# Optimization experiments

Hardware: AMD Instinct MI355X
Metric: run time of the kernel (lower is better)

The kernel has to match this reference:

```python
import jax, jax.numpy as jnp
import numpy as np

B, T, OB, AC, OBL, ACL, W = 2048, 128, 64, 8, 32, 16, 64
DT = 0.05   # spacing of save times
K = 2       # fixed Dopri5 substeps per interval (step size = ode_dt0 = 0.025)


def _mlp2(x, W0, b0, W1, b1):
    # eqx.nn.MLP with depth=1: in -> width (relu) -> out (identity)
    return jax.nn.relu(x @ W0.T + b0) @ W1.T + b1


def setup_inputs() -> dict:
    key = jax.random.key(0)
    ks = jax.random.split(key, 10)
    def lin(k, o, i, scale=1.0):
        return (jax.random.normal(k, (o, i), jnp.float32) * (scale / np.sqrt(i))).astype(jnp.float32)
    return {
        "encW0": lin(ks[0], W, OB), "encb0": jnp.zeros((W,), jnp.float32),
        "encW1": lin(ks[1], OBL, W), "encb1": jnp.zeros((OBL,), jnp.float32),
        "acW0": lin(ks[2], W, AC), "acb0": jnp.zeros((W,), jnp.float32),
        "acW1": lin(ks[3], ACL, W), "acb1": jnp.zeros((ACL,), jnp.float32),
        "dynW0": lin(ks[4], W, OBL + ACL), "dynb0": jnp.zeros((W,), jnp.float32),
        "dynW1": lin(ks[5], OBL, W, 0.5), "dynb1": jnp.zeros((OBL,), jnp.float32),
        "decW0": lin(ks[6], W, OBL), "decb0": jnp.zeros((W,), jnp.float32),
        "decW1": lin(ks[7], OB, W), "decb1": jnp.zeros((OB,), jnp.float32),
        "ob": jax.random.normal(ks[8], (B, OB), jnp.float32),
        "acs": jax.random.normal(ks[9], (B, T, AC), jnp.float32),
        "times": jnp.tile(jnp.arange(T, dtype=jnp.float32) * DT, (B, 1)),
    }


def _dopri5_step(f, t, y, h):
    k1 = f(t, y)
    k2 = f(t + h * (1. / 5.), y + h * ((1. / 5.) * k1))
    k3 = f(t + h * (3. / 10.), y + h * ((3. / 40.) * k1 + (9. / 40.) * k2))
    k4 = f(t + h * (4. / 5.), y + h * ((44. / 45.) * k1 - (56. / 15.) * k2 + (32. / 9.) * k3))
    k5 = f(t + h * (8. / 9.), y + h * ((19372. / 6561.) * k1 - (25360. / 2187.) * k2
                                       + (64448. / 6561.) * k3 - (212. / 729.) * k4))
    k6 = f(t + h, y + h * ((9017. / 3168.) * k1 - (355. / 33.) * k2 + (46732. / 5247.) * k3
                           + (49. / 176.) * k4 - (5103. / 18656.) * k5))
    return y + h * ((35. / 384.) * k1 + (500. / 1113.) * k3 + (125. / 192.) * k4
                    - (2187. / 6784.) * k5 + (11. / 84.) * k6)


def reference(encW0, encb0, encW1, encb1, acW0, acb0, acW1, acb1,
              dynW0, dynb0, dynW1, dynb1, decW0, decb0, decW1, decb1,
              ob, acs, times):
    ac_latents = _mlp2(acs, acW0, acb0, acW1, acb1)   # (B, T, ACL)
    y0 = _mlp2(ob, encW0, encb0, encW1, encb1)        # (B, OBL)

    def single(y0_i, acl_i, t_i):
        n = t_i.shape[0]

        def f(t, y):
            # piecewise-constant action latent: index of save-interval containing t
            idx = jnp.clip(jnp.searchsorted(t_i, t, side='right') - 1, 0, n - 1)
            return _mlp2(jnp.concatenate([y, acl_i[idx]]), dynW0, dynb0, dynW1, dynb1)

        def interval(y, tt):
            t0, t1 = tt
            h = (t1 - t0) / K
            def sub(yc, j):
                return _dopri5_step(f, t0 + j * h, yc, h), None
            y, _ = jax.lax.scan(sub, y, jnp.arange(K, dtype=t_i.dtype))
            return y, y

        _, ys = jax.lax.scan(interval, y0_i, (t_i[:-1], t_i[1:]))
        return jnp.concatenate([y0_i[None], ys], axis=0)   # (T, OBL)

    ys = jax.vmap(single)(y0, ac_latents, times)            # (B, T, OBL)
    return _mlp2(ys, decW0, decb0, decW1, decb1)            # (B, T, OB)
```

## Files before the change

kernel.cpp:

```cpp
#include <hip/hip_runtime.h>

#define NB 2048
#define NT 128

typedef float v2f __attribute__((ext_vector_type(2)));

static __device__ __forceinline__ v2f pkfma(v2f a, v2f b, v2f c) {
#if __has_builtin(__builtin_elementwise_fma)
    return __builtin_elementwise_fma(a, b, c);
#else
    v2f r; r.x = fmaf(a.x, b.x, c.x); r.y = fmaf(a.y, b.y, c.y); return r;
#endif
}
static __device__ __forceinline__ v2f mkv2(float x, float y) { v2f r; r.x = x; r.y = y; return r; }

__global__ __launch_bounds__(256, 4) void acl_kernel(
    const float* __restrict__ acs, const float* __restrict__ acW0,
    const float* __restrict__ acb0, const float* __restrict__ acW1,
    const float* __restrict__ acb1, float* __restrict__ aclout)
{
    __shared__ float sW0[64 * 8];
    __shared__ float sW1[16 * 64];
    __shared__ float sB0[64];
    __shared__ float sB1[16];
    const int tid = threadIdx.x;
    for (int i = tid; i < 64 * 8; i += 256) sW0[i] = acW0[i];
    for (int i = tid; i < 16 * 64; i += 256) sW1[i] = acW1[i];
    if (tid < 64) sB0[tid] = acb0[tid];
    if (tid < 16) sB1[tid] = acb1[tid];
    __syncthreads();

    const int row = blockIdx.x * 256 + tid;
    const float4 x0 = *(const float4*)&acs[row * 8];
    const float4 x1 = *(const float4*)&acs[row * 8 + 4];

    float o[16];
    #pragma unroll
    for (int m = 0; m < 16; ++m) o[m] = sB1[m];

    #pragma unroll
    for (int jc = 0; jc < 16; ++jc) {
        float hq[4];
        #pragma unroll
        for (int u = 0; u < 4; ++u) {
            const int j = jc * 4 + u;
            const float4 wa = *(const float4*)&sW0[j * 8];
            const float4 wb = *(const float4*)&sW0[j * 8 + 4];
            float hv = sB0[j];
            hv = fmaf(x0.x, wa.x, hv); hv = fmaf(x0.y, wa.y, hv);
            hv = fmaf(x0.z, wa.z, hv); hv = fmaf(x0.w, wa.w, hv);
            hv = fmaf(x1.x, wb.x, hv); hv = fmaf(x1.y, wb.y, hv);
            hv = fmaf(x1.z, wb.z, hv); hv = fmaf(x1.w, wb.w, hv);
            hq[u] = fmaxf(hv, 0.f);
        }
        #pragma unroll
        for (int m = 0; m < 16; ++m) {
            const float4 wv = *(const float4*)&sW1[m * 64 + jc * 4];
            o[m] = fmaf(hq[0], wv.x, o[m]);
            o[m] = fmaf(hq[1], wv.y, o[m]);
            o[m] = fmaf(hq[2], wv.z, o[m]);
            o[m] = fmaf(hq[3], wv.w, o[m]);
        }
    }
    float4* op = (float4*)&aclout[row * 16];
    op[0] = make_float4(o[0],  o[1],  o[2],  o[3]);
    op[1] = make_float4(o[4],  o[5],  o[6],  o[7]);
    op[2] = make_float4(o[8],  o[9],  o[10], o[11]);
    op[3] = make_float4(o[12], o[13], o[14], o[15]);
}

__global__ __launch_bounds__(256, 2) void ode_kernel(
    const float* __restrict__ encW0, const float* __restrict__ encb0,
    const float* __restrict__ encW1, const float* __restrict__ encb1,
    const float* __restrict__ dynW0, const float* __restrict__ dynb0,
    const float* __restrict__ dynW1, const float* __restrict__ dynb1,
    const float* __restrict__ ob,    const float* __restrict__ times,
    const float* __restrict__ aclws, float* __restrict__ yio)
{
    __shared__ float sEncW0T[64 * 64];
    __shared__ float sEncW1T[64 * 32];
    __shared__ float sEncB0[64], sEncB1[32];
    __shared__ float xbuf[4][64];
    __shared__ float hbuf[4][64];
    __shared__ float tbuf[4][NT];

    const int tid = threadIdx.x;
    for (int i = tid; i < 64 * 64; i += 256) { int r = i >> 6, c = i & 63; sEncW0T[c * 64 + r] = encW0[i]; }
    for (int i = tid; i < 32 * 64; i += 256) { int r = i >> 6, c = i & 63; sEncW1T[c * 32 + r] = encW1[i]; }
    if (tid < 64) { sEncB0[tid] = encb0[tid]; }
    if (tid < 32) { sEncB1[tid] = encb1[tid]; }

    const int w    = tid >> 6;
    const int lane = tid & 63;
    const int bu   = __builtin_amdgcn_readfirstlane(blockIdx.x * 4 + w);
    const int m    = lane & 31;
    const int jh   = (lane >> 5) * 32;

    float* __restrict__ xb = xbuf[w];
    float* __restrict__ hb = hbuf[w];

    float w0r[48];
    #pragma unroll
    for (int q = 0; q < 12; ++q) *(float4*)&w0r[q * 4] = *(const float4*)&dynW0[lane * 48 + q * 4];
    float w1r[32];
    #pragma unroll
    for (int q = 0; q < 8; ++q)  *(float4*)&w1r[q * 4] = *(const float4*)&dynW1[m * 64 + jh + q * 4];
    const float b0r = dynb0[lane];
    const float b1r = dynb1[m];

    tbuf[w][lane]      = times[bu * NT + lane];
    tbuf[w][64 + lane] = times[bu * NT + 64 + lane];

    __syncthreads();

    auto feval = [&](float hinit) -> float {
        __builtin_amdgcn_wave_barrier();
        float xr[32];
        #pragma unroll
        for (int q = 0; q < 8; ++q) *(float4*)&xr[q * 4] = *(const float4*)&xb[q * 4];
        const v2f* xp  = (const v2f*)xr;
        const v2f* wp  = (const v2f*)w0r;
        v2f a0 = mkv2(hinit, 0.f), a1 = mkv2(0.f, 0.f);
        #pragma unroll
        for (int q = 0; q < 16; q += 2) {
            a0 = pkfma(xp[q],     wp[q],     a0);
            a1 = pkfma(xp[q + 1], wp[q + 1], a1);
        }
        const float hj = fmaxf((a0.x + a1.x) + (a0.y + a1.y), 0.f);
        hb[lane] = hj;
        __builtin_amdgcn_wave_barrier();
        float hr[32];
        #pragma unroll
        for (int q = 0; q < 8; ++q) *(float4*)&hr[q * 4] = *(const float4*)&hb[jh + q * 4];
        const v2f* hp  = (const v2f*)hr;
        const v2f* w1p = (const v2f*)w1r;
        v2f c0 = mkv2(0.f, 0.f), c1 = mkv2(0.f, 0.f);
        #pragma unroll
        for (int q = 0; q < 16; q += 2) {
            c0 = pkfma(hp[q],     w1p[q],     c0);
            c1 = pkfma(hp[q + 1], w1p[q + 1], c1);
        }
        float part = (c0.x + c1.x) + (c0.y + c1.y);
        part += __shfl_xor(part, 32, 64);
        return part + b1r;
    };

    float y;
    {
        xb[lane] = ob[bu * 64 + lane];
        __builtin_amdgcn_wave_barrier();
        float4 xv[16];
        #pragma unroll
        for (int q = 0; q < 16; ++q) xv[q] = *(const float4*)&xb[q * 4];
        float a0 = sEncB0[lane], a1 = 0.f, a2 = 0.f, a3 = 0.f;
        #pragma unroll
        for (int q = 0; q < 16; ++q) {
            a0 = fmaf(xv[q].x, sEncW0T[(q * 4 + 0) * 64 + lane], a0);
            a1 = fmaf(xv[q].y, sEncW0T[(q * 4 + 1) * 64 + lane], a1);
            a2 = fmaf(xv[q].z, sEncW0T[(q * 4 + 2) * 64 + lane], a2);
            a3 = fmaf(xv[q].w, sEncW0T[(q * 4 + 3) * 64 + lane], a3);
        }
        const float hj = fmaxf((a0 + a1) + (a2 + a3), 0.f);
        hb[lane] = hj;
        __builtin_amdgcn_wave_barrier();
        float4 hv[8];
        #pragma unroll
        for (int q = 0; q < 8; ++q) hv[q] = *(const float4*)&hb[jh + q * 4];
        float c0 = 0.f, c1 = 0.f, c2 = 0.f, c3 = 0.f;
        #pragma unroll
        for (int q = 0; q < 8; ++q) {
            c0 = fmaf(hv[q].x, sEncW1T[(jh + q * 4 + 0) * 32 + m], c0);
            c1 = fmaf(hv[q].y, sEncW1T[(jh + q * 4 + 1) * 32 + m], c1);
            c2 = fmaf(hv[q].z, sEncW1T[(jh + q * 4 + 2) * 32 + m], c2);
            c3 = fmaf(hv[q].w, sEncW1T[(jh + q * 4 + 3) * 32 + m], c3);
        }
        float part = (c0 + c1) + (c2 + c3);
        part += __shfl_xor(part, 32, 64);
        y = part + sEncB1[m];
    }

    auto acl_part = [&](const float* __restrict__ ap) -> float {
        float ar[16];
        #pragma unroll
        for (int q = 0; q < 4; ++q) *(float4*)&ar[q * 4] = *(const float4*)&ap[q * 4];
        const v2f* a2 = (const v2f*)ar;
        const v2f* wq = (const v2f*)&w0r[32];
        v2f s0 = mkv2(0.f, 0.f), s1 = mkv2(0.f, 0.f);
        #pragma unroll
        for (int q = 0; q < 8; q += 2) {
            s0 = pkfma(a2[q],     wq[q],     s0);
            s1 = pkfma(a2[q + 1], wq[q + 1], s1);
        }
        const v2f s = s0 + s1;
        return s.x + s.y;
    };

    auto store_y = [&](float yv, int t) {
        if (lane < 32) yio[(size_t)(bu * NT + t) * 64 + lane] = yv;
    };

    float aclPartC = acl_part(aclws + (size_t)(bu * NT) * 16);
    store_y(y, 0);

    for (int i = 0; i < NT - 1; ++i) {
        const float t0v = tbuf[w][i];
        const float t1v = tbuf[w][i + 1];
        const float hh  = (t1v - t0v) * 0.5f;
        const float aclPartN = acl_part(aclws + (size_t)(bu * NT + i + 1) * 16);

        #pragma unroll 1
        for (int sub = 0; sub < 2; ++sub) {
            const float tsub  = t0v + (float)sub * hh;
            const bool  swap6 = (tsub + hh >= t1v);
            const float hpC = b0r + aclPartC;
            const float hp6 = b0r + (swap6 ? aclPartN : aclPartC);

            xb[m] = y;
            const float k1 = feval(hpC);
            xb[m] = fmaf(hh, 0.2f * k1, y);
            const float k2 = feval(hpC);
            xb[m] = fmaf(hh, 0.075f * k1 + 0.225f * k2, y);
            const float k3 = feval(hpC);
            xb[m] = fmaf(hh,
                (float)(44.0/45.0)*k1 + (float)(-56.0/15.0)*k2 + (float)(32.0/9.0)*k3, y);
            const float k4 = feval(hpC);
            xb[m] = fmaf(hh,
                (float)(19372.0/6561.0)*k1 + (float)(-25360.0/2187.0)*k2
              + (float)(64448.0/6561.0)*k3 + (float)(-212.0/729.0)*k4, y);
            const float k5 = feval(hpC);
            xb[m] = fmaf(hh,
                (float)(9017.0/3168.0)*k1 + (float)(-355.0/33.0)*k2
              + (float)(46732.0/5247.0)*k3 + (float)(49.0/176.0)*k4
              + (float)(-5103.0/18656.0)*k5, y);
            const float k6 = feval(hp6);
            y = fmaf(hh,
                (float)(35.0/384.0)*k1 + (float)(500.0/1113.0)*k3
              + (float)(125.0/192.0)*k4 + (float)(-2187.0/6784.0)*k5
              + (float)(11.0/84.0)*k6, y);
        }
        aclPartC = aclPartN;
        store_y(y, i + 1);
    }
}

__global__ __launch_bounds__(256, 2) void dec_kernel(
    const float* __restrict__ decW0, const float* __restrict__ decb0,
    const float* __restrict__ decW1, const float* __restrict__ decb1,
    float* __restrict__ yio)
{
    __shared__ float sW0[64 * 32];
    __shared__ float sW1T[64 * 64];
    __shared__ float sB0[64];
    __shared__ float sB1[64];
    const int tid = threadIdx.x;
    for (int i = tid; i < 64 * 32; i += 256) sW0[i] = decW0[i];
    for (int i = tid; i < 64 * 64; i += 256) { int n = i >> 6, j = i & 63; sW1T[j * 64 + n] = decW1[i]; }
    if (tid < 64) { sB0[tid] = decb0[tid]; sB1[tid] = decb1[tid]; }
    __syncthreads();

    const size_t row = (size_t)blockIdx.x * 256 + tid;
    float* rp = &yio[row * 64];

    float xr[32];
    #pragma unroll
    for (int q = 0; q < 8; ++q) *(float4*)&xr[q * 4] = *(const float4*)&rp[q * 4];

    v2f o2[32];
    #pragma unroll
    for (int n = 0; n < 32; ++n) o2[n] = mkv2(sB1[2 * n], sB1[2 * n + 1]);

    #pragma unroll 4
    for (int j = 0; j < 64; ++j) {
        v2f a0 = mkv2(sB0[j], 0.f), a1 = mkv2(0.f, 0.f);
        #pragma unroll
        for (int q = 0; q < 8; ++q) {
            const float4 wv = *(const float4*)&sW0[j * 32 + q * 4];
            a0 = pkfma(*(const v2f*)&xr[q * 4],     mkv2(wv.x, wv.y), a0);
            a1 = pkfma(*(const v2f*)&xr[q * 4 + 2], mkv2(wv.z, wv.w), a1);
        }
        const float hj = fmaxf((a0.x + a1.x) + (a0.y + a1.y), 0.f);
        const v2f h2 = mkv2(hj, hj);
        #pragma unroll
        for (int q = 0; q < 16; ++q) {
            const float4 wv = *(const float4*)&sW1T[j * 64 + q * 4];
            o2[2 * q]     = pkfma(h2, mkv2(wv.x, wv.y), o2[2 * q]);
            o2[2 * q + 1] = pkfma(h2, mkv2(wv.z, wv.w), o2[2 * q + 1]);
        }
    }

    #pragma unroll
    for (int q = 0; q < 16; ++q)
        *(float4*)&rp[q * 4] = make_float4(o2[2 * q].x, o2[2 * q].y,
                                           o2[2 * q + 1].x, o2[2 * q + 1].y);
}

extern "C" void kernel_launch(void* const* d_in, const int* in_sizes, int n_in,
                              void* d_out, int out_size, void* d_ws, size_t ws_size,
                              hipStream_t stream)
{
    const float* encW0 = (const float*)d_in[0];
    const float* encb0 = (const float*)d_in[1];
    const float* encW1 = (const float*)d_in[2];
    const float* encb1 = (const float*)d_in[3];
    const float* acW0  = (const float*)d_in[4];
    const float* acb0  = (const float*)d_in[5];
    const float* acW1  = (const float*)d_in[6];
    const float* acb1  = (const float*)d_in[7];
    const float* dynW0 = (const float*)d_in[8];
    const float* dynb0 = (const float*)d_in[9];
    const float* dynW1 = (const float*)d_in[10];
    const float* dynb1 = (const float*)d_in[11];
    const float* decW0 = (const float*)d_in[12];
    const float* decb0 = (const float*)d_in[13];
    const float* decW1 = (const float*)d_in[14];
    const float* decb1 = (const float*)d_in[15];
    const float* ob    = (const float*)d_in[16];
    const float* acs   = (const float*)d_in[17];
    const float* times = (const float*)d_in[18];
    float* out = (float*)d_out;
    float* acl = (float*)d_ws;

    acl_kernel<<<(NB * NT) / 256, 256, 0, stream>>>(acs, acW0, acb0, acW1, acb1, acl);
    ode_kernel<<<NB / 4, 256, 0, stream>>>(encW0, encb0, encW1, encb1,
                                           dynW0, dynb0, dynW1, dynb1,
                                           ob, times, acl, out);
    dec_kernel<<<(NB * NT) / 256, 256, 0, stream>>>(decW0, decb0, decW1, decb1, out);
}
```

Baseline: 705.4 us.

## Reformulate Dopri5 stages in hidden-preactivation space with fused W0·W1 matrix

Precomputes M = W0[:, :32]·W1 (64x64) once per block in shared memory and rewrites the RK stages to carry hidden pre-activations. Each stage is now one 64x64 product on the ReLU output, instead of a 64x32 layer followed by a 32x64 layer. The final y update accumulates the weighted hidden activations and applies W1 once per substep. The aim is to cut per-stage LDS round trips and dependent matmuls, at the cost of 64 more registers per lane, a small setup prologue and slightly different floating-point rounding.

```diff
diff --git a/kernel.cpp b/kernel.cpp
--- a/kernel.cpp
+++ b/kernel.cpp
@@ -79,7 +79,10 @@
 {
     __shared__ float sEncW0T[64 * 64];
     __shared__ float sEncW1T[64 * 32];
-    __shared__ float sEncB0[64], sEncB1[32];
+    __shared__ float sW0s[64 * 32];
+    __shared__ float sW1T[64 * 32];
+    __shared__ float sM[64 * 64];
+    __shared__ float sEncB0[64], sEncB1[32], sB1d[32];
     __shared__ float xbuf[4][64];
     __shared__ float hbuf[4][64];
     __shared__ float tbuf[4][NT];
@@ -87,14 +90,38 @@
     const int tid = threadIdx.x;
     for (int i = tid; i < 64 * 64; i += 256) { int r = i >> 6, c = i & 63; sEncW0T[c * 64 + r] = encW0[i]; }
     for (int i = tid; i < 32 * 64; i += 256) { int r = i >> 6, c = i & 63; sEncW1T[c * 32 + r] = encW1[i]; }
+    for (int i = tid; i < 64 * 32; i += 256) { int j = i >> 5, mm = i & 31; sW0s[i] = dynW0[j * 48 + mm]; }
+    for (int i = tid; i < 64 * 32; i += 256) { int c = i >> 5, mm = i & 31; sW1T[i] = dynW1[mm * 64 + c]; }
     if (tid < 64) { sEncB0[tid] = encb0[tid]; }
-    if (tid < 32) { sEncB1[tid] = encb1[tid]; }
+    if (tid < 32) { sEncB1[tid] = encb1[tid]; sB1d[tid] = dynb1[tid]; }
+    __syncthreads();
+
+    {
+        const int j  = tid >> 2;
+        const int cg = (tid & 3) * 16;
+        float4 wr[8];
+        #pragma unroll
+        for (int q = 0; q < 8; ++q) wr[q] = *(const float4*)&sW0s[j * 32 + q * 4];
+        #pragma unroll 2
+        for (int k = 0; k < 16; ++k) {
+            const int c = cg + k;
+            v2f s0 = mkv2(0.f, 0.f), s1 = mkv2(0.f, 0.f);
+            #pragma unroll
+            for (int q = 0; q < 8; ++q) {
+                const float4 t4 = *(const float4*)&sW1T[c * 32 + q * 4];
+                s0 = pkfma(mkv2(t4.x, t4.y), mkv2(wr[q].x, wr[q].y), s0);
+                s1 = pkfma(mkv2(t4.z, t4.w), mkv2(wr[q].z, wr[q].w), s1);
+            }
+            sM[j * 64 + c] = (s0.x + s1.x) + (s0.y + s1.y);
+        }
+    }
+    __syncthreads();
 
     const int w    = tid >> 6;
     const int lane = tid & 63;
     const int bu   = __builtin_amdgcn_readfirstlane(blockIdx.x * 4 + w);
     const int m    = lane & 31;
-    const int jh   = (lane >> 5) * 32;
+    const int H    = lane & 32;
 
     float* __restrict__ xb = xbuf[w];
     float* __restrict__ hb = hbuf[w];
@@ -104,45 +131,55 @@
     for (int q = 0; q < 12; ++q) *(float4*)&w0r[q * 4] = *(const float4*)&dynW0[lane * 48 + q * 4];
     float w1r[32];
     #pragma unroll
-    for (int q = 0; q < 8; ++q)  *(float4*)&w1r[q * 4] = *(const float4*)&dynW1[m * 64 + jh + q * 4];
+    for (int q = 0; q < 8; ++q)  *(float4*)&w1r[q * 4] = *(const float4*)&dynW1[m * 64 + H + q * 4];
+    float Ma[32], Mb[32];
+    #pragma unroll
+    for (int q = 0; q < 8; ++q) *(float4*)&Ma[q * 4] = *(const float4*)&sM[lane * 64 + H + q * 4];
+    #pragma unroll
+    for (int q = 0; q < 8; ++q) *(float4*)&Mb[q * 4] = *(const float4*)&sM[(lane ^ 32) * 64 + H + q * 4];
     const float b0r = dynb0[lane];
     const float b1r = dynb1[m];
 
+    float vj;
+    {
+        v2f s0 = mkv2(0.f, 0.f), s1 = mkv2(0.f, 0.f);
+        const v2f* wp = (const v2f*)w0r;
+        const v2f* bp = (const v2f*)sB1d;
+        #pragma unroll
+        for (int q = 0; q < 16; q += 2) {
+            s0 = pkfma(bp[q],     wp[q],     s0);
+            s1 = pkfma(bp[q + 1], wp[q + 1], s1);
+        }
+        vj = (s0.x + s1.x) + (s0.y + s1.y);
+    }
+
     tbuf[w][lane]      = times[bu * NT + lane];
     tbuf[w][64 + lane] = times[bu * NT + 64 + lane];
-
-    __syncthreads();
-
-    auto feval = [&](float hinit) -> float {
+    __builtin_amdgcn_wave_barrier();
+
+    auto gproj = [&](float hsv) -> float {
         __builtin_amdgcn_wave_barrier();
-        float xr[32];
-        #pragma unroll
-        for (int q = 0; q < 8; ++q) *(float4*)&xr[q * 4] = *(const float4*)&xb[q * 4];
-        const v2f* xp  = (const v2f*)xr;
-        const v2f* wp  = (const v2f*)w0r;
-        v2f a0 = mkv2(hinit, 0.f), a1 = mkv2(0.f, 0.f);
-        #pragma unroll
-        for (int q = 0; q < 16; q += 2) {
-            a0 = pkfma(xp[q],     wp[q],     a0);
-            a1 = pkfma(xp[q + 1], wp[q + 1], a1);
-        }
-        const float hj = fmaxf((a0.x + a1.x) + (a0.y + a1.y), 0.f);
-        hb[lane] = hj;
+        hb[lane] = hsv;
         __builtin_amdgcn_wave_barrier();
         float hr[32];
         #pragma unroll
-        for (int q = 0; q < 8; ++q) *(float4*)&hr[q * 4] = *(const float4*)&hb[jh + q * 4];
-        const v2f* hp  = (const v2f*)hr;
-        const v2f* w1p = (const v2f*)w1r;
-        v2f c0 = mkv2(0.f, 0.f), c1 = mkv2(0.f, 0.f);
+        for (int q = 0; q < 8; ++q) *(float4*)&hr[q * 4] = *(const float4*)&hb[H + q * 4];
+        const v2f* hp = (const v2f*)hr;
+        const v2f* ma = (const v2f*)Ma;
+        const v2f* mb = (const v2f*)Mb;
+        v2f o0 = mkv2(0.f, 0.f), o1 = mkv2(0.f, 0.f);
+        v2f p0 = mkv2(0.f, 0.f), p1 = mkv2(0.f, 0.f);
         #pragma unroll
         for (int q = 0; q < 16; q += 2) {
-            c0 = pkfma(hp[q],     w1p[q],     c0);
-            c1 = pkfma(hp[q + 1], w1p[q + 1], c1);
-        }
-        float part = (c0.x + c1.x) + (c0.y + c1.y);
-        part += __shfl_xor(part, 32, 64);
-        return part + b1r;
+            o0 = pkfma(hp[q],     ma[q],     o0);
+            o1 = pkfma(hp[q + 1], ma[q + 1], o1);
+            p0 = pkfma(hp[q],     mb[q],     p0);
+            p1 = pkfma(hp[q + 1], mb[q + 1], p1);
+        }
+        const float own = (o0.x + o1.x) + (o0.y + o1.y);
+        float par = (p0.x + p1.x) + (p0.y + p1.y);
+        par = __shfl_xor(par, 32, 64);
+        return own + par + vj;
     };
 
     float y;
@@ -165,14 +202,14 @@
         __builtin_amdgcn_wave_barrier();
         float4 hv[8];
         #pragma unroll
-        for (int q = 0; q < 8; ++q) hv[q] = *(const float4*)&hb[jh + q * 4];
+        for (int q = 0; q < 8; ++q) hv[q] = *(const float4*)&hb[H + q * 4];
         float c0 = 0.f, c1 = 0.f, c2 = 0.f, c3 = 0.f;
         #pragma unroll
         for (int q = 0; q < 8; ++q) {
-            c0 = fmaf(hv[q].x, sEncW1T[(jh + q * 4 + 0) * 32 + m], c0);
-            c1 = fmaf(hv[q].y, sEncW1T[(jh + q * 4 + 1) * 32 + m], c1);
-            c2 = fmaf(hv[q].z, sEncW1T[(jh + q * 4 + 2) * 32 + m], c2);
-            c3 = fmaf(hv[q].w, sEncW1T[(jh + q * 4 + 3) * 32 + m], c3);
+            c0 = fmaf(hv[q].x, sEncW1T[(H + q * 4 + 0) * 32 + m], c0);
+            c1 = fmaf(hv[q].y, sEncW1T[(H + q * 4 + 1) * 32 + m], c1);
+            c2 = fmaf(hv[q].z, sEncW1T[(H + q * 4 + 2) * 32 + m], c2);
+            c3 = fmaf(hv[q].w, sEncW1T[(H + q * 4 + 3) * 32 + m], c3);
         }
         float part = (c0 + c1) + (c2 + c3);
         part += __shfl_xor(part, 32, 64);
@@ -212,31 +249,77 @@
         for (int sub = 0; sub < 2; ++sub) {
             const float tsub  = t0v + (float)sub * hh;
             const bool  swap6 = (tsub + hh >= t1v);
-            const float hpC = b0r + aclPartC;
-            const float hp6 = b0r + (swap6 ? aclPartN : aclPartC);
-
+
+            __builtin_amdgcn_wave_barrier();
             xb[m] = y;
-            const float k1 = feval(hpC);
-            xb[m] = fmaf(hh, 0.2f * k1, y);
-            const float k2 = feval(hpC);
-            xb[m] = fmaf(hh, 0.075f * k1 + 0.225f * k2, y);
-            const float k3 = feval(hpC);
-            xb[m] = fmaf(hh,
-                (float)(44.0/45.0)*k1 + (float)(-56.0/15.0)*k2 + (float)(32.0/9.0)*k3, y);
-            const float k4 = feval(hpC);
-            xb[m] = fmaf(hh,
-                (float)(19372.0/6561.0)*k1 + (float)(-25360.0/2187.0)*k2
-              + (float)(64448.0/6561.0)*k3 + (float)(-212.0/729.0)*k4, y);
-            const float k5 = feval(hpC);
-            xb[m] = fmaf(hh,
-                (float)(9017.0/3168.0)*k1 + (float)(-355.0/33.0)*k2
-              + (float)(46732.0/5247.0)*k3 + (float)(49.0/176.0)*k4
-              + (float)(-5103.0/18656.0)*k5, y);
-            const float k6 = feval(hp6);
-            y = fmaf(hh,
-                (float)(35.0/384.0)*k1 + (float)(500.0/1113.0)*k3
-              + (float)(125.0/192.0)*k4 + (float)(-2187.0/6784.0)*k5
-              + (float)(11.0/84.0)*k6, y);
+            __builtin_amdgcn_wave_barrier();
+            float a1v;
+            {
+                float xr[32];
+                #pragma unroll
+                for (int q = 0; q < 8; ++q) *(float4*)&xr[q * 4] = *(const float4*)&xb[q * 4];
+                const v2f* xp = (const v2f*)xr;
+                const v2f* wp = (const v2f*)w0r;
+                v2f s0 = mkv2(b0r + aclPartC, 0.f), s1 = mkv2(0.f, 0.f);
+                #pragma unroll
+                for (int q = 0; q < 16; q += 2) {
+                    s0 = pkfma(xp[q],     wp[q],     s0);
+                    s1 = pkfma(xp[q + 1], wp[q + 1], s1);
+                }
+                a1v = (s0.x + s1.x) + (s0.y + s1.y);
+            }
+
+            const float h1 = fmaxf(a1v, 0.f);
+            const float g1 = hh * gproj(h1);
+            const float h2 = fmaxf(fmaf(0.2f, g1, a1v), 0.f);
+            const float g2 = hh * gproj(h2);
+            const float h3 = fmaxf(fmaf(0.075f, g1, fmaf(0.225f, g2, a1v)), 0.f);
+            const float g3 = hh * gproj(h3);
+            const float h4 = fmaxf(
+                fmaf((float)(44.0/45.0), g1,
+                fmaf((float)(-56.0/15.0), g2,
+                fmaf((float)(32.0/9.0), g3, a1v))), 0.f);
+            const float g4 = hh * gproj(h4);
+            const float h5 = fmaxf(
+                fmaf((float)(19372.0/6561.0), g1,
+                fmaf((float)(-25360.0/2187.0), g2,
+                fmaf((float)(64448.0/6561.0), g3,
+                fmaf((float)(-212.0/729.0), g4, a1v)))), 0.f);
+            const float g5 = hh * gproj(h5);
+            float a6v =
+                fmaf((float)(9017.0/3168.0), g1,
+                fmaf((float)(-355.0/33.0), g2,
+                fmaf((float)(46732.0/5247.0), g3,
+                fmaf((float)(49.0/176.0), g4,
+                fmaf((float)(-5103.0/18656.0), g5, a1v)))));
+            a6v += swap6 ? (aclPartN - aclPartC) : 0.f;
+            const float h6 = fmaxf(a6v, 0.f);
+
+            float ha = (float)(35.0/384.0) * h1;
+            ha = fmaf((float)(500.0/1113.0),   h3, ha);
+            ha = fmaf((float)(125.0/192.0),    h4, ha);
+            ha = fmaf((float)(-2187.0/6784.0), h5, ha);
+            ha = fmaf((float)(11.0/84.0),      h6, ha);
+
+            __builtin_amdgcn_wave_barrier();
+            hb[lane] = ha;
+            __builtin_amdgcn_wave_barrier();
+            {
+                float hr[32];
+                #pragma unroll
+                for (int q = 0; q < 8; ++q) *(float4*)&hr[q * 4] = *(const float4*)&hb[H + q * 4];
+                const v2f* hp  = (const v2f*)hr;
+                const v2f* w1p = (const v2f*)w1r;
+                v2f c0 = mkv2(0.f, 0.f), c1 = mkv2(0.f, 0.f);
+                #pragma unroll
+                for (int q = 0; q < 16; q += 2) {
+                    c0 = pkfma(hp[q],     w1p[q],     c0);
+                    c1 = pkfma(hp[q + 1], w1p[q + 1], c1);
+                }
+                float part = (c0.x + c1.x) + (c0.y + c1.y);
+                part += __shfl_xor(part, 32, 64);
+                y = fmaf(hh, part + b1r, y);
+            }
         }
         aclPartC = aclPartN;
         store_y(y, i + 1);
```

Result: faster. 614.1 us (-12.9%).
